# Optimization experiments

Measured on AMD Instinct MI355X. Metric: run time of the kernel, lower is better.

Reference implementation:

```python
import jax, jax.numpy as jnp
import numpy as np

B, SENSORY, UNITS, MOTOR = 4096, 64, 128, 32
ODE_UNFOLDS = 6
EPSILON = 1e-8
ELAPSED_TIME = 1.0


def setup_inputs() -> dict:
    key = jax.random.key(0)
    ks = jax.random.split(key, 16)
    u = lambda k, shape, lo, hi: jax.random.uniform(k, shape, jnp.float32, lo, hi)
    return {
        "inputs": jax.random.normal(ks[0], (B, SENSORY), jnp.float32),
        "state": jax.random.normal(ks[1], (B, UNITS), jnp.float32),
        "gleak": u(ks[2], (UNITS,), 0.001, 1.0),
        "vleak": u(ks[3], (UNITS,), -0.2, 0.2),
        "cm": u(ks[4], (UNITS,), 0.4, 0.6),
        "sigma": u(ks[5], (UNITS, UNITS), 3.0, 8.0),
        "mu": u(ks[6], (UNITS, UNITS), 0.3, 0.8),
        "w": u(ks[7], (UNITS, UNITS), 0.001, 1.0),
        "erev": jnp.sign(jax.random.normal(ks[8], (UNITS, UNITS), jnp.float32)),
        "sensory_sigma": u(ks[9], (SENSORY, UNITS), 3.0, 8.0),
        "sensory_mu": u(ks[10], (SENSORY, UNITS), 0.3, 0.8),
        "sensory_w": u(ks[11], (SENSORY, UNITS), 0.001, 1.0),
        "sensory_erev": jnp.sign(jax.random.normal(ks[12], (SENSORY, UNITS), jnp.float32)),
        "input_w": jnp.ones((SENSORY,), jnp.float32),
        "input_b": jnp.zeros((SENSORY,), jnp.float32),
        "output_w": jnp.ones((MOTOR,), jnp.float32),
        "output_b": jnp.zeros((MOTOR,), jnp.float32),
        "sparsity_mask": jax.random.randint(ks[13], (UNITS, UNITS), 0, 2) > 0,
        "sensory_sparsity_mask": jax.random.randint(ks[14], (SENSORY, UNITS), 0, 2) > 0,
    }


def reference(inputs, state, gleak, vleak, cm, sigma, mu, w, erev,
              sensory_sigma, sensory_mu, sensory_w, sensory_erev,
              input_w, input_b, output_w, output_b,
              sparsity_mask, sensory_sparsity_mask):
    mask = sparsity_mask.astype(jnp.float32)
    smask = sensory_sparsity_mask.astype(jnp.float32)

    # input mapping (affine)
    x = inputs * input_w + input_b  # [B, sensory]

    # sensory synapse activation: [B, sensory, units]
    sens_act = sensory_w * jax.nn.sigmoid(sensory_sigma * (x[:, :, None] - sensory_mu)) * smask
    w_num_sensory = jnp.sum(sens_act * sensory_erev, axis=1)  # [B, units]
    w_den_sensory = jnp.sum(sens_act, axis=1)                 # [B, units]

    cm_t = cm / (ELAPSED_TIME / ODE_UNFOLDS)  # [units]

    def step(v_pre, _):
        # [B, units, units] broadcasted synapse activation
        wa = w * jax.nn.sigmoid(sigma * (v_pre[:, :, None] - mu)) * mask
        w_num = jnp.sum(wa * erev, axis=1) + w_num_sensory
        w_den = jnp.sum(wa, axis=1) + w_den_sensory
        numerator = cm_t * v_pre + gleak * vleak + w_num
        denominator = cm_t + gleak + w_den
        return numerator / (denominator + EPSILON), None

    next_state, _ = jax.lax.scan(step, state, None, length=ODE_UNFOLDS)

    # output mapping: slice motor neurons, affine
    out = next_state[:, :MOTOR] * output_w + output_b
    return out, next_state
```

## Files before the change

kernel.cpp:

```cpp
#include <hip/hip_runtime.h>

#define BATCH    4096
#define SENS     64
#define UNITS    128
#define MOTOR_N  32
#define UNFOLDS  6
#define NB       4
#define ROWS_PER_BLOCK 16
#define NBLOCKS  (BATCH / ROWS_PER_BLOCK)
#define NGROUPS  (ROWS_PER_BLOCK / NB)

#define LOG2E 1.4426950408889634f

__device__ __forceinline__ float fast_exp2(float x) { return __builtin_amdgcn_exp2f(x); }
__device__ __forceinline__ float fast_rcp(float x)  { return __builtin_amdgcn_rcpf(x); }

__global__ __launch_bounds__(1024)
__attribute__((amdgpu_waves_per_eu(4, 4)))
void ltc_fused(
    const float* __restrict__ inputs,  const float* __restrict__ state,
    const float* __restrict__ gleak,   const float* __restrict__ vleak,
    const float* __restrict__ cm,
    const float* __restrict__ sigma,   const float* __restrict__ mu,
    const float* __restrict__ w,       const float* __restrict__ erev,
    const float* __restrict__ s_sigma, const float* __restrict__ s_mu,
    const float* __restrict__ s_w,     const float* __restrict__ s_erev,
    const float* __restrict__ input_w, const float* __restrict__ input_b,
    const float* __restrict__ output_w,const float* __restrict__ output_b,
    const int*   __restrict__ mask,    const int* __restrict__ s_mask,
    float* __restrict__ out, float* __restrict__ next_state)
{
    __shared__ float x_lds[NB][SENS];
    __shared__ float v_lds[NB][UNITS];
    __shared__ float pn[NB][8][UNITS];
    __shared__ float pd[NB][8][UNITS];

    const int t = threadIdx.x;
    const int u = t & (UNITS - 1);
    const int c = t >> 7;

    float rgl[16], rgb[16], rws[16];
#pragma unroll
    for (int k = 0; k < 16; ++k) {
        int idx = (c * 16 + k) * UNITS + u;
        float sg = sigma[idx] * LOG2E;
        float wv = w[idx] * (mask[idx] != 0 ? 1.0f : 0.0f);
        rgl[k] = -sg;
        rgb[k] = sg * mu[idx];
        rws[k] = wv * erev[idx];
    }
    float sgl[8], sgb[8], sws[8];
#pragma unroll
    for (int j = 0; j < 8; ++j) {
        int idx = (c * 8 + j) * UNITS + u;
        float sg = s_sigma[idx] * LOG2E;
        float wv = s_w[idx] * (s_mask[idx] != 0 ? 1.0f : 0.0f);
        sgl[j] = -sg;
        sgb[j] = sg * s_mu[idx];
        sws[j] = wv * s_erev[idx];
    }
#pragma unroll
    for (int k = 0; k < 16; ++k)
        asm volatile("" : "+v"(rgl[k]), "+v"(rgb[k]), "+v"(rws[k]));
#pragma unroll
    for (int j = 0; j < 8; ++j)
        asm volatile("" : "+v"(sgl[j]), "+v"(sgb[j]), "+v"(sws[j]));

    const bool red = (t < NB * UNITS);
    const int  rb  = t >> 7;
    const int  ru  = u;
    const float cmt = cm[ru] * 6.0f;
    const float nb0 = gleak[ru] * vleak[ru];
    const float db0 = cmt + gleak[ru] + 1e-8f;

    for (int g = 0; g < NGROUPS; ++g) {
        const int b0 = blockIdx.x * ROWS_PER_BLOCK + g * NB;

        if (t < NB * SENS) {
            int b = t >> 6, s = t & 63;
            x_lds[b][s] = inputs[(b0 + b) * SENS + s] * input_w[s] + input_b[s];
        }
        float vcur = 0.f, nbase = 0.f, dbase = 0.f;
        if (red) {
            vcur = state[(b0 + rb) * UNITS + ru];
            v_lds[rb][ru] = vcur;
        }
        __syncthreads();

#pragma unroll 1
        for (int b = 0; b < NB; ++b) {
            float n = 0.f, d = 0.f;
            const float4* xp = (const float4*)&x_lds[b][c * 8];
            float4 xa = xp[0], xb = xp[1];
            float xs[8] = {xa.x, xa.y, xa.z, xa.w, xb.x, xb.y, xb.z, xb.w};
#pragma unroll
            for (int j = 0; j < 8; ++j) {
                float e = fast_exp2(fmaf(sgl[j], xs[j], sgb[j]));
                float r = fast_rcp(1.0f + e);
                n = fmaf(sws[j], r, n);
                d = fmaf(fabsf(sws[j]), r, d);
            }
            pn[b][c][u] = n;
            pd[b][c][u] = d;
        }
        __syncthreads();

        if (red) {
            float n = nb0, d = db0;
#pragma unroll
            for (int cc = 0; cc < 8; ++cc) {
                n += pn[rb][cc][ru];
                d += pd[rb][cc][ru];
            }
            nbase = n; dbase = d;
        }
        __syncthreads();

#pragma unroll 1
        for (int step = 0; step < UNFOLDS; ++step) {
#pragma unroll 1
            for (int b = 0; b < NB; ++b) {
                float n = 0.f, d = 0.f;
                const float4* vp = (const float4*)&v_lds[b][c * 16];
#pragma unroll
                for (int q = 0; q < 4; ++q) {
                    float4 v4 = vp[q];
                    const float* vf = (const float*)&v4;
#pragma unroll
                    for (int jj = 0; jj < 4; ++jj) {
                        int k = q * 4 + jj;
                        float e = fast_exp2(fmaf(rgl[k], vf[jj], rgb[k]));
                        float r = fast_rcp(1.0f + e);
                        n = fmaf(rws[k], r, n);
                        d = fmaf(fabsf(rws[k]), r, d);
                    }
                }
                pn[b][c][u] = n;
                pd[b][c][u] = d;
            }
            __syncthreads();

            if (red) {
                float n = nbase, d = dbase;
#pragma unroll
                for (int cc = 0; cc < 8; ++cc) {
                    n += pn[rb][cc][ru];
                    d += pd[rb][cc][ru];
                }
                vcur = fmaf(cmt, vcur, n) * fast_rcp(d);
                v_lds[rb][ru] = vcur;
            }
            __syncthreads();
        }

        if (red) {
            int row = b0 + rb;
            next_state[row * UNITS + ru] = vcur;
            if (ru < MOTOR_N)
                out[row * MOTOR_N + ru] = vcur * output_w[ru] + output_b[ru];
        }
        __syncthreads();
    }
}

extern "C" void kernel_launch(void* const* d_in, const int* in_sizes, int n_in,
                              void* d_out, int out_size, void* d_ws, size_t ws_size,
                              hipStream_t stream) {
    const float* inputs   = (const float*)d_in[0];
    const float* state    = (const float*)d_in[1];
    const float* gleak    = (const float*)d_in[2];
    const float* vleak    = (const float*)d_in[3];
    const float* cm       = (const float*)d_in[4];
    const float* sigma    = (const float*)d_in[5];
    const float* mu       = (const float*)d_in[6];
    const float* w        = (const float*)d_in[7];
    const float* erev     = (const float*)d_in[8];
    const float* s_sigma  = (const float*)d_in[9];
    const float* s_mu     = (const float*)d_in[10];
    const float* s_w      = (const float*)d_in[11];
    const float* s_erev   = (const float*)d_in[12];
    const float* input_w  = (const float*)d_in[13];
    const float* input_b  = (const float*)d_in[14];
    const float* output_w = (const float*)d_in[15];
    const float* output_b = (const float*)d_in[16];
    const int*   mask     = (const int*)d_in[17];
    const int*   s_mask   = (const int*)d_in[18];

    float* out        = (float*)d_out;
    float* next_state = out + (size_t)BATCH * MOTOR_N;

    ltc_fused<<<NBLOCKS, 1024, 0, stream>>>(
        inputs, state, gleak, vleak, cm, sigma, mu, w, erev,
        s_sigma, s_mu, s_w, s_erev, input_w, input_b, output_w, output_b,
        mask, s_mask, out, next_state);
}
```

Before: 198.5 us.

## Reduce partial sums with wave shuffles, double-buffer state, and pack weights as bf16

The thread mapping changes so the 8 threads sharing a unit are adjacent lanes. Their partial sums are reduced with xor shuffles, replacing the LDS partial arrays and the separate reduction phase, which removes one barrier per ODE step. Sensory terms are now computed once for all 16 rows up front, the state buffer is double-buffered and padded against bank conflicts, and the recurrent weights are packed as bf16 to free registers. The waves-per-EU attribute is dropped. The bf16 weights lower precision and may exceed tolerance, and there is an odd redundant store into x_lds.

```diff
diff --git a/kernel.cpp b/kernel.cpp
--- a/kernel.cpp
+++ b/kernel.cpp
@@ -9,14 +9,23 @@
 #define ROWS_PER_BLOCK 16
 #define NBLOCKS  (BATCH / ROWS_PER_BLOCK)
 #define NGROUPS  (ROWS_PER_BLOCK / NB)
+#define VP 140
+#define XP 68
 
 #define LOG2E 1.4426950408889634f
 
 __device__ __forceinline__ float fast_exp2(float x) { return __builtin_amdgcn_exp2f(x); }
 __device__ __forceinline__ float fast_rcp(float x)  { return __builtin_amdgcn_rcpf(x); }
+__device__ __forceinline__ unsigned f2bf(float x) {
+    unsigned v = __float_as_uint(x);
+    v += 0x7fffu + ((v >> 16) & 1u);
+    return v >> 16;
+}
+__device__ __forceinline__ float bf_lo(unsigned p) { return __uint_as_float(p << 16); }
+__device__ __forceinline__ float bf_hi(unsigned p) { return __uint_as_float(p & 0xffff0000u); }
+__device__ __forceinline__ int vpad(int j) { return j + ((j >> 5) << 2); }
 
 __global__ __launch_bounds__(1024)
-__attribute__((amdgpu_waves_per_eu(4, 4)))
 void ltc_fused(
     const float* __restrict__ inputs,  const float* __restrict__ state,
     const float* __restrict__ gleak,   const float* __restrict__ vleak,
@@ -30,136 +39,160 @@
     const int*   __restrict__ mask,    const int* __restrict__ s_mask,
     float* __restrict__ out, float* __restrict__ next_state)
 {
-    __shared__ float x_lds[NB][SENS];
-    __shared__ float v_lds[NB][UNITS];
-    __shared__ float pn[NB][8][UNITS];
-    __shared__ float pd[NB][8][UNITS];
+    __shared__ __align__(16) float x_lds[ROWS_PER_BLOCK][XP];
+    __shared__ float nb_lds[ROWS_PER_BLOCK][UNITS];
+    __shared__ float db_lds[ROWS_PER_BLOCK][UNITS];
+    __shared__ __align__(16) float v_lds[2][NB][VP];
 
     const int t = threadIdx.x;
-    const int u = t & (UNITS - 1);
-    const int c = t >> 7;
-
-    float rgl[16], rgb[16], rws[16];
-#pragma unroll
-    for (int k = 0; k < 16; ++k) {
-        int idx = (c * 16 + k) * UNITS + u;
-        float sg = sigma[idx] * LOG2E;
-        float wv = w[idx] * (mask[idx] != 0 ? 1.0f : 0.0f);
-        rgl[k] = -sg;
-        rgb[k] = sg * mu[idx];
-        rws[k] = wv * erev[idx];
-    }
-    float sgl[8], sgb[8], sws[8];
-#pragma unroll
-    for (int j = 0; j < 8; ++j) {
-        int idx = (c * 8 + j) * UNITS + u;
-        float sg = s_sigma[idx] * LOG2E;
-        float wv = s_w[idx] * (s_mask[idx] != 0 ? 1.0f : 0.0f);
-        sgl[j] = -sg;
-        sgb[j] = sg * s_mu[idx];
-        sws[j] = wv * s_erev[idx];
+    const int u = t >> 3;
+    const int c = t & 7;
+    const int vread = c * 16 + ((c >> 1) << 2);
+    const int xread = c * 8  + ((c >> 2) << 2);
+
+    const float cmt = cm[u] * 6.0f;
+    const float glv = gleak[u];
+    const float nb0 = glv * vleak[u];
+    const float db0 = cmt + glv + 1e-8f;
+
+    {
+        const int r = t >> 6, s = t & 63;
+        x_lds[r][vpad(s) == s + ((s >> 5) << 2) ? s + ((s >> 5) << 2) : 0] =
+            0.0f;
+        x_lds[r][s + ((s >> 5) << 2)] =
+            inputs[(blockIdx.x * ROWS_PER_BLOCK + r) * SENS + s] * input_w[s] + input_b[s];
+    }
+
+    float sgl[8], sgb[8];
+    unsigned swsp[4];
+#pragma unroll
+    for (int k2 = 0; k2 < 4; ++k2) {
+        float wt[2];
+#pragma unroll
+        for (int e = 0; e < 2; ++e) {
+            int k = k2 * 2 + e;
+            int idx = (c * 8 + k) * UNITS + u;
+            float sg = s_sigma[idx] * LOG2E;
+            float wv = s_w[idx] * (s_mask[idx] != 0 ? 1.0f : 0.0f);
+            sgl[k] = -sg;
+            sgb[k] = sg * s_mu[idx];
+            wt[e]  = wv * s_erev[idx];
+        }
+        swsp[k2] = (f2bf(wt[1]) << 16) | f2bf(wt[0]);
+    }
+    __syncthreads();
+
+#pragma unroll 1
+    for (int row = 0; row < ROWS_PER_BLOCK; ++row) {
+        const float4* xp = (const float4*)&x_lds[row][xread];
+        float4 xa = xp[0], xb = xp[1];
+        float xs[8] = {xa.x, xa.y, xa.z, xa.w, xb.x, xb.y, xb.z, xb.w};
+        float nsum = 0.f, dsum = 0.f;
+#pragma unroll
+        for (int k = 0; k < 8; ++k) {
+            float e  = fast_exp2(fmaf(sgl[k], xs[k], sgb[k]));
+            float r  = fast_rcp(1.0f + e);
+            float ws = (k & 1) ? bf_hi(swsp[k >> 1]) : bf_lo(swsp[k >> 1]);
+            nsum = fmaf(ws, r, nsum);
+            dsum = fmaf(fabsf(ws), r, dsum);
+        }
+        nsum += __shfl_xor(nsum, 1, 8);
+        nsum += __shfl_xor(nsum, 2, 8);
+        nsum += __shfl_xor(nsum, 4, 8);
+        dsum += __shfl_xor(dsum, 1, 8);
+        dsum += __shfl_xor(dsum, 2, 8);
+        dsum += __shfl_xor(dsum, 4, 8);
+        if (c == 0) {
+            nb_lds[row][u] = nb0 + nsum;
+            db_lds[row][u] = db0 + dsum;
+        }
+    }
+
+    float rgl[16], rgb[16];
+    unsigned rwsp[8];
+#pragma unroll
+    for (int k2 = 0; k2 < 8; ++k2) {
+        float wt[2];
+#pragma unroll
+        for (int e = 0; e < 2; ++e) {
+            int k = k2 * 2 + e;
+            int idx = (c * 16 + k) * UNITS + u;
+            float sg = sigma[idx] * LOG2E;
+            float wv = w[idx] * (mask[idx] != 0 ? 1.0f : 0.0f);
+            rgl[k] = -sg;
+            rgb[k] = sg * mu[idx];
+            wt[e]  = wv * erev[idx];
+        }
+        rwsp[k2] = (f2bf(wt[1]) << 16) | f2bf(wt[0]);
     }
 #pragma unroll
     for (int k = 0; k < 16; ++k)
-        asm volatile("" : "+v"(rgl[k]), "+v"(rgb[k]), "+v"(rws[k]));
-#pragma unroll
-    for (int j = 0; j < 8; ++j)
-        asm volatile("" : "+v"(sgl[j]), "+v"(sgb[j]), "+v"(sws[j]));
-
-    const bool red = (t < NB * UNITS);
-    const int  rb  = t >> 7;
-    const int  ru  = u;
-    const float cmt = cm[ru] * 6.0f;
-    const float nb0 = gleak[ru] * vleak[ru];
-    const float db0 = cmt + gleak[ru] + 1e-8f;
-
+        asm volatile("" : "+v"(rgl[k]), "+v"(rgb[k]));
+#pragma unroll
+    for (int k2 = 0; k2 < 8; ++k2)
+        asm volatile("" : "+v"(rwsp[k2]));
+
+    __syncthreads();
+
+#pragma unroll 1
     for (int g = 0; g < NGROUPS; ++g) {
         const int b0 = blockIdx.x * ROWS_PER_BLOCK + g * NB;
-
-        if (t < NB * SENS) {
-            int b = t >> 6, s = t & 63;
-            x_lds[b][s] = inputs[(b0 + b) * SENS + s] * input_w[s] + input_b[s];
-        }
-        float vcur = 0.f, nbase = 0.f, dbase = 0.f;
-        if (red) {
-            vcur = state[(b0 + rb) * UNITS + ru];
-            v_lds[rb][ru] = vcur;
+        if (t < NB * UNITS) {
+            int b = t >> 7, j = t & 127;
+            v_lds[0][b][vpad(j)] = state[(b0 + b) * UNITS + j];
         }
         __syncthreads();
 
-#pragma unroll 1
-        for (int b = 0; b < NB; ++b) {
-            float n = 0.f, d = 0.f;
-            const float4* xp = (const float4*)&x_lds[b][c * 8];
-            float4 xa = xp[0], xb = xp[1];
-            float xs[8] = {xa.x, xa.y, xa.z, xa.w, xb.x, xb.y, xb.z, xb.w};
-#pragma unroll
-            for (int j = 0; j < 8; ++j) {
-                float e = fast_exp2(fmaf(sgl[j], xs[j], sgb[j]));
-                float r = fast_rcp(1.0f + e);
-                n = fmaf(sws[j], r, n);
-                d = fmaf(fabsf(sws[j]), r, d);
-            }
-            pn[b][c][u] = n;
-            pd[b][c][u] = d;
-        }
-        __syncthreads();
-
-        if (red) {
-            float n = nb0, d = db0;
-#pragma unroll
-            for (int cc = 0; cc < 8; ++cc) {
-                n += pn[rb][cc][ru];
-                d += pd[rb][cc][ru];
-            }
-            nbase = n; dbase = d;
-        }
-        __syncthreads();
-
+        float vc[NB];
+#pragma unroll
+        for (int b = 0; b < NB; ++b) vc[b] = v_lds[0][b][vpad(u)];
+
+        int p = 0;
 #pragma unroll 1
         for (int step = 0; step < UNFOLDS; ++step) {
-#pragma unroll 1
+#pragma unroll
             for (int b = 0; b < NB; ++b) {
-                float n = 0.f, d = 0.f;
-                const float4* vp = (const float4*)&v_lds[b][c * 16];
+                const float4* vp4 = (const float4*)&v_lds[p][b][vread];
+                float nsum = 0.f, dsum = 0.f;
 #pragma unroll
                 for (int q = 0; q < 4; ++q) {
-                    float4 v4 = vp[q];
+                    float4 v4 = vp4[q];
                     const float* vf = (const float*)&v4;
 #pragma unroll
                     for (int jj = 0; jj < 4; ++jj) {
                         int k = q * 4 + jj;
-                        float e = fast_exp2(fmaf(rgl[k], vf[jj], rgb[k]));
-                        float r = fast_rcp(1.0f + e);
-                        n = fmaf(rws[k], r, n);
-                        d = fmaf(fabsf(rws[k]), r, d);
+                        float e  = fast_exp2(fmaf(rgl[k], vf[jj], rgb[k]));
+                        float r  = fast_rcp(1.0f + e);
+                        float ws = (k & 1) ? bf_hi(rwsp[k >> 1]) : bf_lo(rwsp[k >> 1]);
+                        nsum = fmaf(ws, r, nsum);
+                        dsum = fmaf(fabsf(ws), r, dsum);
                     }
                 }
-                pn[b][c][u] = n;
-                pd[b][c][u] = d;
+                nsum += __shfl_xor(nsum, 1, 8);
+                nsum += __shfl_xor(nsum, 2, 8);
+                nsum += __shfl_xor(nsum, 4, 8);
+                dsum += __shfl_xor(dsum, 1, 8);
+                dsum += __shfl_xor(dsum, 2, 8);
+                dsum += __shfl_xor(dsum, 4, 8);
+                const int row = g * NB + b;
+                float vnew = fmaf(cmt, vc[b], nsum + nb_lds[row][u])
+                           * fast_rcp(dsum + db_lds[row][u]);
+                vc[b] = vnew;
+                if (c == 0) v_lds[p ^ 1][b][vpad(u)] = vnew;
             }
             __syncthreads();
-
-            if (red) {
-                float n = nbase, d = dbase;
-#pragma unroll
-                for (int cc = 0; cc < 8; ++cc) {
-                    n += pn[rb][cc][ru];
-                    d += pd[rb][cc][ru];
-                }
-                vcur = fmaf(cmt, vcur, n) * fast_rcp(d);
-                v_lds[rb][ru] = vcur;
+            p ^= 1;
+        }
+
+        if (c == 0) {
+#pragma unroll
+            for (int b = 0; b < NB; ++b) {
+                const int row = b0 + b;
+                next_state[row * UNITS + u] = vc[b];
+                if (u < MOTOR_N)
+                    out[row * MOTOR_N + u] = vc[b] * output_w[u] + output_b[u];
             }
-            __syncthreads();
-        }
-
-        if (red) {
-            int row = b0 + rb;
-            next_state[row * UNITS + ru] = vcur;
-            if (ru < MOTOR_N)
-                out[row * MOTOR_N + ru] = vcur * output_w[ru] + output_b[ru];
-        }
-        __syncthreads();
+        }
     }
 }
 
```

Result: slower. 222.5 us (+12.1%).
